# Kernel optimization log

Measured on AMD Instinct MI355X. Metric: run time of the kernel, lower is better.

## Reference

```python
import jax, jax.numpy as jnp
import numpy as np

B, D, C = 8192, 2048, 1000
EPS32 = float(np.finfo(np.float32).eps)      # torch clamp_probs uses finfo.eps
LOG_2PI = float(np.log(2.0 * np.pi))
GAMMA = float(1.0 / np.exp(100.0))           # lerp at global_step=0 -> start_val = 1/exp(start_rho)


def setup_inputs() -> dict:
    key = jax.random.key(0)
    k = jax.random.split(key, 6)
    feature = jax.random.normal(k[0], (B, D), jnp.float32)
    target = jax.random.randint(k[1], (B,), 0, C)
    eps = jax.random.normal(k[2], (B, D), jnp.float32)
    # y_project: Linear(C, D) -> weight [D, C], bias [D]
    y_w = jax.random.normal(k[3], (D, C), jnp.float32) * 0.02
    y_b = jnp.zeros((D,), jnp.float32)
    # cls_project: Linear(D, C) -> weight [C, D], bias [C]
    # small weights + positive bias keep Categorical probs positive (torch would
    # clamp negatives to eps; we replicate the clamp but avoid degenerate NaNs)
    cls_w = jax.random.normal(k[4], (C, D), jnp.float32) * 0.001
    cls_b = jnp.ones((C,), jnp.float32) * 5.0
    return dict(feature=feature, y_w=y_w, y_b=y_b, cls_w=cls_w, cls_b=cls_b,
                eps=eps, target=target)


def reference(feature, y_w, y_b, cls_w, cls_b, eps, target):
    # z = m.sample() : identity-covariance MVN sample, detached (torch .sample())
    z = jax.lax.stop_gradient(feature + eps)                      # [B, D]

    # y_emb = y_project(one_hot(target)) == gather of weight columns + bias
    y_emb = jnp.take(y_w, target, axis=1).T + y_b                 # [B, D]

    # Categorical(probs=cls_project(z)): normalize, clamp, log
    probs_raw = z @ cls_w.T + cls_b                               # [B, C]
    p = probs_raw / jnp.sum(probs_raw, axis=-1, keepdims=True)
    logits = jnp.log(jnp.clip(p, EPS32, 1.0 - EPS32))             # [B, C]

    # identity-covariance MVN log_prob in closed form
    const = 0.5 * D * LOG_2PI
    h1 = 0.5 * jnp.sum((z - feature) ** 2, axis=-1) + const       # -m.log_prob(z)
    h2 = 0.5 * jnp.sum((z - y_emb) ** 2, axis=-1) + const         # -y_emb_d.log_prob(z)
    h3 = -jnp.take_along_axis(logits, target[:, None], axis=1)[:, 0]

    rex = h2 - h1
    loss = jnp.mean(jnp.float32(GAMMA) * rex + h3)
    return logits, loss
```

## Files before the change

### kernel.cpp

```cpp
#include <hip/hip_runtime.h>
#include <hip/hip_bf16.h>

#define B_ROWS 8192
#define D_DIM  2048
#define C_DIM  1000
#define C_PAD  1024

#define EPS32   1.1920928955078125e-07f

typedef __attribute__((ext_vector_type(8))) short short8;
typedef __attribute__((ext_vector_type(4))) float f32x4;

#define GLOAD_LDS16(gptr, lptr) \
  __builtin_amdgcn_global_load_lds((const __attribute__((address_space(1))) void*)(gptr), \
                                   (__attribute__((address_space(3))) void*)(lptr), 16, 0, 0)

__device__ inline unsigned short f2bf(float x) {
  union { __hip_bfloat16 b; unsigned short u; } cv;
  cv.b = __float2bfloat16(x);
  return cv.u;
}

__device__ inline float wave_red(float v) {
#pragma unroll
  for (int off = 32; off > 0; off >>= 1) v += __shfl_down(v, off, 64);
  return v;
}

__global__ __launch_bounds__(256) void cast_w(const float* __restrict__ cls_w,
                                              __hip_bfloat16* __restrict__ clsw_bf) {
  int j = (blockIdx.x * 256 + threadIdx.x) * 8;
  int row = j >> 11;
  int col = j & 2047;
  union { unsigned short u[8]; uint4 v; } pk;
  if (row < C_DIM) {
    const float* src = cls_w + (size_t)row * D_DIM + col;
#pragma unroll
    for (int i2 = 0; i2 < 8; ++i2) pk.u[i2] = f2bf(src[i2]);
  } else {
#pragma unroll
    for (int i2 = 0; i2 < 8; ++i2) pk.u[i2] = 0;
  }
  *(uint4*)((unsigned short*)clsw_bf + j) = pk.v;
}

__global__ __launch_bounds__(256) void gemm_fz(const float* __restrict__ feature,
                                               const float* __restrict__ eps,
                                               const __hip_bfloat16* __restrict__ Bt,
                                               const float* __restrict__ cls_b,
                                               float* __restrict__ out) {
  __shared__ __align__(16) __hip_bfloat16 sA[128 * 64];
  __shared__ __align__(16) __hip_bfloat16 sB[128 * 64];
  const int tid = threadIdx.x;
  const int m0 = blockIdx.x * 128;
  const int n0 = blockIdx.y * 128;
  const int w = tid >> 6, lane = tid & 63;
  const int wm = (w & 1) * 64, wn = (w >> 1) * 64;
  const int l15 = lane & 15, quad = lane >> 4;

  f32x4 acc[4][4] = {};

  for (int k0 = 0; k0 < D_DIM; k0 += 64) {
    float4 fa[4], fb[4], ea[4], eb[4];
#pragma unroll
    for (int i = 0; i < 4; ++i) {
      int j = i * 256 + tid;
      int row = j >> 3;
      int cc = (j & 7) ^ (row & 7);
      const float* sF = feature + (size_t)(m0 + row) * D_DIM + k0 + cc * 8;
      const float* sE = eps     + (size_t)(m0 + row) * D_DIM + k0 + cc * 8;
      fa[i] = *(const float4*)sF;
      fb[i] = *(const float4*)(sF + 4);
      ea[i] = *(const float4*)sE;
      eb[i] = *(const float4*)(sE + 4);
    }
#pragma unroll
    for (int i = 0; i < 4; ++i) {
      int j = i * 256 + tid;
      int row = j >> 3;
      int cc = (j & 7) ^ (row & 7);
      const __hip_bfloat16* srcB = Bt + (size_t)(n0 + row) * D_DIM + k0 + cc * 8;
      GLOAD_LDS16(srcB, &sB[j * 8]);
    }
#pragma unroll
    for (int i = 0; i < 4; ++i) {
      int j = i * 256 + tid;
      union { unsigned short u[8]; uint4 v; } pk;
      pk.u[0] = f2bf(fa[i].x + ea[i].x);
      pk.u[1] = f2bf(fa[i].y + ea[i].y);
      pk.u[2] = f2bf(fa[i].z + ea[i].z);
      pk.u[3] = f2bf(fa[i].w + ea[i].w);
      pk.u[4] = f2bf(fb[i].x + eb[i].x);
      pk.u[5] = f2bf(fb[i].y + eb[i].y);
      pk.u[6] = f2bf(fb[i].z + eb[i].z);
      pk.u[7] = f2bf(fb[i].w + eb[i].w);
      *(uint4*)&sA[j * 8] = pk.v;
    }
    __syncthreads();
#pragma unroll
    for (int kk = 0; kk < 64; kk += 32) {
      const int ccr = (kk >> 3) + quad;
      short8 af[4], bfr[4];
#pragma unroll
      for (int i = 0; i < 4; ++i) {
        int r = wm + i * 16 + l15;
        af[i] = *(const short8*)&sA[(r * 8 + (ccr ^ (r & 7))) * 8];
      }
#pragma unroll
      for (int jn = 0; jn < 4; ++jn) {
        int r = wn + jn * 16 + l15;
        bfr[jn] = *(const short8*)&sB[(r * 8 + (ccr ^ (r & 7))) * 8];
      }
#pragma unroll
      for (int i = 0; i < 4; ++i)
#pragma unroll
        for (int jn = 0; jn < 4; ++jn)
          acc[i][jn] = __builtin_amdgcn_mfma_f32_16x16x32_bf16(af[i], bfr[jn], acc[i][jn], 0, 0, 0);
    }
    __syncthreads();
  }

#pragma unroll
  for (int i = 0; i < 4; ++i) {
    int row = m0 + wm + i * 16 + quad * 4;
#pragma unroll
    for (int jn = 0; jn < 4; ++jn) {
      int col = n0 + wn + jn * 16 + l15;
      if (col < C_DIM) {
        float bias = cls_b[col];
#pragma unroll
        for (int r = 0; r < 4; ++r)
          out[(size_t)(row + r) * C_DIM + col] = acc[i][jn][r] + bias;
      }
    }
  }
}

__global__ __launch_bounds__(256) void rownorm(float* __restrict__ out,
                                               const int* __restrict__ target,
                                               float* __restrict__ rowloss) {
  int b = blockIdx.x * 4 + (threadIdx.x >> 6);
  int lane = threadIdx.x & 63;
  float* row = out + (size_t)b * C_DIM;

  float v[16];
  float s = 0.f;
#pragma unroll
  for (int k = 0; k < 4; ++k) {
    int c = k * 256 + lane * 4;
    if (c + 3 < C_DIM) {
      float4 f = *(const float4*)(row + c);
      v[k * 4 + 0] = f.x; v[k * 4 + 1] = f.y; v[k * 4 + 2] = f.z; v[k * 4 + 3] = f.w;
    } else {
#pragma unroll
      for (int i = 0; i < 4; ++i) v[k * 4 + i] = (c + i < C_DIM) ? row[c + i] : 0.f;
    }
    s += v[k * 4 + 0] + v[k * 4 + 1] + v[k * 4 + 2] + v[k * 4 + 3];
  }
  s = wave_red(s);
  float inv = 1.0f / __shfl(s, 0, 64);
  int t = target[b];

#pragma unroll
  for (int k = 0; k < 4; ++k) {
    int c = k * 256 + lane * 4;
    float lg[4];
#pragma unroll
    for (int i = 0; i < 4; ++i) {
      float p = v[k * 4 + i] * inv;
      p = fminf(fmaxf(p, EPS32), 1.0f - EPS32);
      lg[i] = __logf(p);
      if (c + i == t) rowloss[b] = -lg[i];
    }
    if (c + 3 < C_DIM) {
      *(float4*)(row + c) = make_float4(lg[0], lg[1], lg[2], lg[3]);
    } else {
#pragma unroll
      for (int i = 0; i < 4; ++i) if (c + i < C_DIM) row[c + i] = lg[i];
    }
  }
}

__global__ __launch_bounds__(256) void finalize(const float* __restrict__ rowloss,
                                                float* __restrict__ out_loss) {
  int tid = threadIdx.x;
  float s = 0.f;
  for (int i = tid; i < B_ROWS; i += 256) s += rowloss[i];
  s = wave_red(s);
  __shared__ float sm[4];
  if ((tid & 63) == 0) sm[tid >> 6] = s;
  __syncthreads();
  if (tid == 0) out_loss[0] = (sm[0] + sm[1] + sm[2] + sm[3]) * (1.0f / B_ROWS);
}

extern "C" void kernel_launch(void* const* d_in, const int* in_sizes, int n_in,
                              void* d_out, int out_size, void* d_ws, size_t ws_size,
                              hipStream_t stream) {
  const float* feature = (const float*)d_in[0];
  const float* cls_w   = (const float*)d_in[3];
  const float* cls_b   = (const float*)d_in[4];
  const float* eps     = (const float*)d_in[5];
  const int*   target  = (const int*)d_in[6];
  float* out = (float*)d_out;
  float* out_loss = out + (size_t)B_ROWS * C_DIM;

  char* ws = (char*)d_ws;
  __hip_bfloat16* clsw_bf = (__hip_bfloat16*)ws;
  float*          rowloss = (float*)(ws + 4194304);

  cast_w<<<dim3(1024), 256, 0, stream>>>(cls_w, clsw_bf);
  gemm_fz<<<dim3(B_ROWS / 128, C_PAD / 128), 256, 0, stream>>>(feature, eps, clsw_bf, cls_b, out);
  rownorm<<<dim3(B_ROWS / 4), 256, 0, stream>>>(out, target, rowloss);
  finalize<<<dim3(1), 256, 0, stream>>>(rowloss, out_loss);
}
```

Before: 270.6 us.

## Double-buffer GEMM shared memory to overlap next-tile loads with MFMA compute

The GEMM main loop now uses two LDS buffers for A and B. It issues the global loads for tile k+1 (feature/eps into registers, the cls_w slice via direct-to-LDS loads) before computing on tile k, then converts and writes the A tile afterwards. This leaves one barrier per iteration instead of two. Per-thread base pointers are hoisted out of the loop, and launch_bounds requests 2 blocks per CU. The cost is doubled LDS use (64KB per block) and more live registers, which may limit occupancy.

Measured after the change: 256.0 us. -5.4%, faster.

```diff
diff --git a/kernel.cpp b/kernel.cpp
--- a/kernel.cpp
+++ b/kernel.cpp
@@ -44,13 +44,15 @@
   *(uint4*)((unsigned short*)clsw_bf + j) = pk.v;
 }
 
-__global__ __launch_bounds__(256) void gemm_fz(const float* __restrict__ feature,
-                                               const float* __restrict__ eps,
-                                               const __hip_bfloat16* __restrict__ Bt,
-                                               const float* __restrict__ cls_b,
-                                               float* __restrict__ out) {
-  __shared__ __align__(16) __hip_bfloat16 sA[128 * 64];
-  __shared__ __align__(16) __hip_bfloat16 sB[128 * 64];
+__global__ __launch_bounds__(256, 2) void gemm_fz(const float* __restrict__ feature,
+                                                  const float* __restrict__ eps,
+                                                  const __hip_bfloat16* __restrict__ Bt,
+                                                  const float* __restrict__ cls_b,
+                                                  float* __restrict__ out) {
+  __shared__ __align__(16) __hip_bfloat16 sA0[128 * 64];
+  __shared__ __align__(16) __hip_bfloat16 sA1[128 * 64];
+  __shared__ __align__(16) __hip_bfloat16 sB0[128 * 64];
+  __shared__ __align__(16) __hip_bfloat16 sB1[128 * 64];
   const int tid = threadIdx.x;
   const int m0 = blockIdx.x * 128;
   const int n0 = blockIdx.y * 128;
@@ -58,33 +60,37 @@
   const int wm = (w & 1) * 64, wn = (w >> 1) * 64;
   const int l15 = lane & 15, quad = lane >> 4;
 
+  const float* Fb[4]; const float* Eb[4]; const __hip_bfloat16* Bb[4]; int slot[4];
+#pragma unroll
+  for (int i = 0; i < 4; ++i) {
+    int j = i * 256 + tid;
+    int row = j >> 3;
+    int cc = (j & 7) ^ (row & 7);
+    Fb[i] = feature + (size_t)(m0 + row) * D_DIM + cc * 8;
+    Eb[i] = eps     + (size_t)(m0 + row) * D_DIM + cc * 8;
+    Bb[i] = Bt      + (size_t)(n0 + row) * D_DIM + cc * 8;
+    slot[i] = j * 8;
+  }
+
   f32x4 acc[4][4] = {};
-
-  for (int k0 = 0; k0 < D_DIM; k0 += 64) {
-    float4 fa[4], fb[4], ea[4], eb[4];
+  float4 fa[4], fb[4], ea[4], eb[4];
+
+  auto LOADA = [&](int k0) {
 #pragma unroll
     for (int i = 0; i < 4; ++i) {
-      int j = i * 256 + tid;
-      int row = j >> 3;
-      int cc = (j & 7) ^ (row & 7);
-      const float* sF = feature + (size_t)(m0 + row) * D_DIM + k0 + cc * 8;
-      const float* sE = eps     + (size_t)(m0 + row) * D_DIM + k0 + cc * 8;
-      fa[i] = *(const float4*)sF;
-      fb[i] = *(const float4*)(sF + 4);
-      ea[i] = *(const float4*)sE;
-      eb[i] = *(const float4*)(sE + 4);
-    }
+      fa[i] = *(const float4*)(Fb[i] + k0);
+      fb[i] = *(const float4*)(Fb[i] + k0 + 4);
+      ea[i] = *(const float4*)(Eb[i] + k0);
+      eb[i] = *(const float4*)(Eb[i] + k0 + 4);
+    }
+  };
+  auto GLOADB = [&](__hip_bfloat16* sB, int k0) {
+#pragma unroll
+    for (int i = 0; i < 4; ++i) GLOAD_LDS16(Bb[i] + k0, &sB[slot[i]]);
+  };
+  auto WRITEA = [&](__hip_bfloat16* sA) {
 #pragma unroll
     for (int i = 0; i < 4; ++i) {
-      int j = i * 256 + tid;
-      int row = j >> 3;
-      int cc = (j & 7) ^ (row & 7);
-      const __hip_bfloat16* srcB = Bt + (size_t)(n0 + row) * D_DIM + k0 + cc * 8;
-      GLOAD_LDS16(srcB, &sB[j * 8]);
-    }
-#pragma unroll
-    for (int i = 0; i < 4; ++i) {
-      int j = i * 256 + tid;
       union { unsigned short u[8]; uint4 v; } pk;
       pk.u[0] = f2bf(fa[i].x + ea[i].x);
       pk.u[1] = f2bf(fa[i].y + ea[i].y);
@@ -94,9 +100,10 @@
       pk.u[5] = f2bf(fb[i].y + eb[i].y);
       pk.u[6] = f2bf(fb[i].z + eb[i].z);
       pk.u[7] = f2bf(fb[i].w + eb[i].w);
-      *(uint4*)&sA[j * 8] = pk.v;
-    }
-    __syncthreads();
+      *(uint4*)&sA[slot[i]] = pk.v;
+    }
+  };
+  auto COMPUTE = [&](const __hip_bfloat16* sA, const __hip_bfloat16* sB) {
 #pragma unroll
     for (int kk = 0; kk < 64; kk += 32) {
       const int ccr = (kk >> 3) + quad;
@@ -117,7 +124,27 @@
         for (int jn = 0; jn < 4; ++jn)
           acc[i][jn] = __builtin_amdgcn_mfma_f32_16x16x32_bf16(af[i], bfr[jn], acc[i][jn], 0, 0, 0);
     }
+  };
+
+  LOADA(0);
+  GLOADB(sB0, 0);
+  WRITEA(sA0);
+  __syncthreads();
+
+  __hip_bfloat16 *cA = sA0, *cB = sB0, *nA = sA1, *nB = sB1;
+  for (int k0 = 0; k0 < D_DIM; k0 += 64) {
+    const int kn = k0 + 64;
+    const bool pf = kn < D_DIM;
+    if (pf) {
+      LOADA(kn);
+      GLOADB(nB, kn);
+    }
+    COMPUTE(cA, cB);
+    if (pf) WRITEA(nA);
     __syncthreads();
+    __hip_bfloat16* t;
+    t = cA; cA = nA; nA = t;
+    t = cB; cB = nB; nB = t;
   }
 
 #pragma unroll
```
